# Optimization experiments

Measured on AMD Instinct MI355X. Metric: run time of the kernel, lower is better.

## Reference

```python
import jax, jax.numpy as jnp
import numpy as np

PAD = 7                 # init padding
T = 2 * PAD + 1         # T_side_dense = 15 shifts per axis
LAMDA = 1.0             # init lamda
EPS = 1e-16             # hardcoded epsilon in the torch loss body


def _joint_hist(x_out, x_tf_out):
    # Equivalent of F.conv2d(x_out.permute(1,0,2,3), weight=x_tf_out.permute(1,0,2,3), padding=PAD)
    # expressed as T*T shifted matmuls (correlation / cost-volume form).
    bn, k, h, w = x_out.shape
    A = jnp.transpose(x_out, (1, 0, 2, 3))      # (k, bn, h, w)  conv "input"
    B = jnp.transpose(x_tf_out, (1, 0, 2, 3))   # (k, bn, h, w)  conv "weight"
    A_pad = jnp.pad(A, ((0, 0), (0, 0), (PAD, PAD), (PAD, PAD)))

    def step(carry, s):
        dy, dx = s // T, s % T
        sl = jax.lax.dynamic_slice(A_pad, (0, 0, dy, dx), (k, bn, h, w))
        # p[n, o] at this shift = sum_{c,y,x} A_pad[n,c,y+dy,x+dx] * B[o,c,y,x]
        return carry, jnp.einsum('nchw,ochw->no', sl, B)

    _, p = jax.lax.scan(step, None, jnp.arange(T * T))
    # (T*T, k, k) -> (T, T, k, k); matches torch p_i_j.permute(2, 3, 0, 1)
    return p.reshape(T, T, k, k)


def reference(x_out, x_tf_out):
    p = _joint_hist(x_out, x_tf_out)
    # shift to positive; min is detached in torch -> stop_gradient
    p = p - jax.lax.stop_gradient(p.min()) + EPS
    # normalize per shift over the (k, k) joint
    p = p / p.sum(axis=(2, 3), keepdims=True)
    # symmetrize
    p = (p + jnp.swapaxes(p, 2, 3)) / 2.0
    p_i = p.sum(axis=2, keepdims=True)   # (T, T, 1, k) marginal (broadcasts like repeat)
    p_j = p.sum(axis=3, keepdims=True)   # (T, T, k, 1) marginal
    loss = (-p * (jnp.log(p + EPS)
                  - LAMDA * jnp.log(p_i + EPS)
                  - LAMDA * jnp.log(p_j + EPS))).sum() / (T * T)
    return loss


def setup_inputs() -> dict:
    key = jax.random.key(0)
    k1, k2 = jax.random.split(key)
    bn, k, h, w = 16, 10, 224, 224
    # simplex over axis=1 is asserted by the torch module -> use softmax
    x_out = jax.nn.softmax(jax.random.normal(k1, (bn, k, h, w), dtype=jnp.float32), axis=1)
    x_tf_out = jax.nn.softmax(jax.random.normal(k2, (bn, k, h, w), dtype=jnp.float32), axis=1)
    return {"x_out": x_out, "x_tf_out": x_tf_out}
```

## Files before the change

kernel.cpp:

```cpp
#include <hip/hip_runtime.h>
#include <stdint.h>
#include <math.h>


#define PADV 7
#define TS 15
#define KCLS 10
#define HH 224
#define WW 224
#define MD 160
#define NCELL (MD*MD)
#define NBLK 512
#define TY 7
#define BSTRIDE 232
#define BPH 240
#define ADW 120
#define LEPS 1e-16

typedef __attribute__((ext_vector_type(4))) float f32x4;
typedef __attribute__((ext_vector_type(8))) short bf16x8;

__device__ __forceinline__ unsigned short f2bf(float f) {
  union { float f; uint32_t u; } v; v.f = f;
  return (unsigned short)((v.u + 0x7FFFu + ((v.u >> 16) & 1u)) >> 16);
}

__device__ __forceinline__ void glds16(const unsigned short* g, unsigned short* l) {
  __builtin_amdgcn_global_load_lds(
      (const __attribute__((address_space(1))) unsigned int*)g,
      (__attribute__((address_space(3))) unsigned int*)l, 16, 0, 0);
}

struct U5 { uint32_t u[5]; };

__device__ __forceinline__ void ldA5(const uint32_t* p, U5& d) {
  uint4 t;
  __builtin_memcpy(&t, p, 16);
  d.u[0] = t.x; d.u[1] = t.y; d.u[2] = t.z; d.u[3] = t.w;
  d.u[4] = p[4];
}

#define BPREP_BLOCKS 4350
#define APREP_BLOCKS 4200
__global__ __launch_bounds__(256)
void prep(const float* __restrict__ xo, const float* __restrict__ xt,
          unsigned short* __restrict__ bp, uint32_t* __restrict__ ap) {
  if (blockIdx.x < BPREP_BLOCKS) {
    const int idx   = blockIdx.x * 256 + threadIdx.x;
    const int rowid = idx / 29;
    const int chunk = idx - rowid * 29;
    const int x0    = chunk * 8;
    const int yy    = rowid % BPH;
    const int cls   = rowid / BPH;
    const int row   = yy - PADV;
    union { unsigned short h[8]; uint4 v; } out;
    if (row >= 0 && row < HH && x0 < WW) {
      const float* src = xt + ((size_t)cls * HH + row) * WW + x0;
#pragma unroll
      for (int j = 0; j < 8; ++j) out.h[j] = f2bf(src[j]);
    } else {
      out.v = make_uint4(0u, 0u, 0u, 0u);
    }
    *(uint4*)(bp + (size_t)rowid * BSTRIDE + x0) = out.v;
  } else {
    const int idx   = (blockIdx.x - BPREP_BLOCKS) * 256 + threadIdx.x;
    const int rowid = idx / 30;
    const int wg    = idx - rowid * 30;
    const float* src = xo + (size_t)rowid * WW;
    float e[8];
#pragma unroll
    for (int j = 0; j < 8; ++j) {
      const int x = 8 * wg + j - PADV;
      e[j] = (x >= 0 && x < WW) ? src[x] : 0.f;
    }
    union { uint32_t u[4]; uint4 v; } o;
#pragma unroll
    for (int k = 0; k < 4; ++k)
      o.u[k] = (uint32_t)f2bf(e[2 * k]) | ((uint32_t)f2bf(e[2 * k + 1]) << 16);
    *(uint4*)(ap + (size_t)rowid * ADW + 4 * wg) = o.v;
  }
}

__global__ __launch_bounds__(256, 2)
void corr_gemm(const uint32_t* __restrict__ apad,
               const unsigned short* __restrict__ bpad,
               float* __restrict__ partials) {
  __shared__ __align__(16) unsigned short ldsB[KCLS * 16 * BSTRIDE];

  const int tid  = threadIdx.x;
  const int bid  = blockIdx.x;
  const int b    = bid >> 5;
  const int y0   = (bid & 31) * TY;

  const int lane = tid & 63;
  const int wv   = tid >> 6;
  const int wm   = wv & 1;
  const int wn   = wv >> 1;
  const int quad = lane >> 4;
  const int l15  = lane & 15;

  const int shA    = (l15 & 1) << 4;
  const int laneWd = quad * 4 + (l15 >> 1);

  f32x4 acc[5][5];
#pragma unroll
  for (int i = 0; i < 5; ++i)
#pragma unroll
    for (int j = 0; j < 5; ++j) acc[i][j] = (f32x4){0.f, 0.f, 0.f, 0.f};

  const unsigned short* Bb = bpad + (size_t)b * KCLS * BPH * BSTRIDE;
  const uint32_t* Abase = apad + ((size_t)(b * KCLS + wm * 5) * HH) * ADW;

  for (int pr = wv; pr < 15 * KCLS; pr += 4) {
    const int r15  = pr / KCLS;
    const int o    = pr - r15 * KCLS;
    const int yy   = y0 + r15;
    const int slot = (y0 - PADV + r15) & 15;
    if (lane < 29)
      glds16(Bb + ((size_t)o * BPH + yy) * BSTRIDE + lane * 8,
             ldsB + (o * 16 + slot) * BSTRIDE);
  }

  U5 bufA[5], bufB[5];
#pragma unroll
  for (int mi = 0; mi < 5; ++mi)
    ldA5(Abase + ((size_t)mi * HH + y0) * ADW + laneWd, bufA[mi]);

  __syncthreads();

  auto step = [&](int t, U5 (&use)[5], U5 (&pre)[5]) {
    const int ydiv = t / 7;
    const int xc   = t - 7 * ydiv;
    const int y    = y0 + ydiv;

    if (xc == 0) {
      const int yy   = y + 8 + PADV;
      const int slot = (y + 8) & 15;
      for (int ro = wv; ro < KCLS; ro += 4) {
        if (lane < 29)
          glds16(Bb + ((size_t)ro * BPH + yy) * BSTRIDE + lane * 8,
                 ldsB + (ro * 16 + slot) * BSTRIDE);
      }
    }

    if (t < 48) {
      const int t1    = t + 1;
      const int ydiv1 = t1 / 7;
      const int xc1   = t1 - 7 * ydiv1;
      const int y1    = y0 + ydiv1;
#pragma unroll
      for (int mi = 0; mi < 5; ++mi)
        ldA5(Abase + ((size_t)mi * HH + y1) * ADW + xc1 * 16 + laneWd, pre[mi]);
    }

    bf16x8 afrag[5];
#pragma unroll
    for (int mi = 0; mi < 5; ++mi) {
      union { uint32_t u[4]; bf16x8 v; } cv;
      cv.u[0] = __builtin_amdgcn_alignbit(use[mi].u[1], use[mi].u[0], shA);
      cv.u[1] = __builtin_amdgcn_alignbit(use[mi].u[2], use[mi].u[1], shA);
      cv.u[2] = __builtin_amdgcn_alignbit(use[mi].u[3], use[mi].u[2], shA);
      cv.u[3] = __builtin_amdgcn_alignbit(use[mi].u[4], use[mi].u[3], shA);
      afrag[mi] = cv.v;
    }

    const int x0    = xc * 32;
    const int slotB = (y + PADV - l15) & 15;
    bf16x8 bfrag[5];
#pragma unroll
    for (int ni = 0; ni < 5; ++ni) {
      const int to = wn * 5 + ni;
      bfrag[ni] = *(const bf16x8*)(ldsB + (to * 16 + slotB) * BSTRIDE + x0 + quad * 8);
    }

#pragma unroll
    for (int mi = 0; mi < 5; ++mi)
#pragma unroll
      for (int ni = 0; ni < 5; ++ni)
        acc[mi][ni] = __builtin_amdgcn_mfma_f32_16x16x32_bf16(
            afrag[mi], bfrag[ni], acc[mi][ni], 0, 0, 0);

    if (xc == 6 && t < 48) __syncthreads();
  };

  for (int ph = 0; ph < 25; ++ph) {
    const int t0 = 2 * ph;
    step(t0, bufA, bufB);
    if (t0 + 1 < 49) step(t0 + 1, bufB, bufA);
  }

  float* outp = partials + (size_t)bid * NCELL;
#pragma unroll
  for (int mi = 0; mi < 5; ++mi)
#pragma unroll
    for (int ni = 0; ni < 5; ++ni) {
      const int mrow = (wm * 5 + mi) * 16 + quad * 4;
      const int ncol = (wn * 5 + ni) * 16 + l15;
#pragma unroll
      for (int r = 0; r < 4; ++r)
        outp[(size_t)(mrow + r) * MD + ncol] = acc[mi][ni][r];
    }
}

__global__ __launch_bounds__(256)
void reduce_all(const float* __restrict__ partials, float* __restrict__ Cout,
                float* __restrict__ mins, float* __restrict__ dout) {
  const int c = blockIdx.x * 256 + threadIdx.x;
  if (c == 0) dout[0] = 0.f;
  double s0 = 0.0, s1 = 0.0, s2 = 0.0, s3 = 0.0;
  const float* base = partials + c;
  for (int p = 0; p < NBLK; p += 4) {
    s0 += (double)base[(size_t)(p + 0) * NCELL];
    s1 += (double)base[(size_t)(p + 1) * NCELL];
    s2 += (double)base[(size_t)(p + 2) * NCELL];
    s3 += (double)base[(size_t)(p + 3) * NCELL];
  }
  const float sf = (float)((s0 + s1) + (s2 + s3));
  Cout[c] = sf;
  const int m  = c / MD;
  const int nn = c - m * MD;
  const bool valid = ((m & 15) < TS) && ((nn & 15) < TS);
  __shared__ float red[256];
  red[threadIdx.x] = valid ? sf : 3.4e38f;
  __syncthreads();
  for (int st = 128; st > 0; st >>= 1) {
    if (threadIdx.x < st)
      red[threadIdx.x] = fminf(red[threadIdx.x], red[threadIdx.x + st]);
    __syncthreads();
  }
  if (threadIdx.x == 0) mins[blockIdx.x] = red[0];
}

__global__ __launch_bounds__(128)
void loss_kernel(const float* __restrict__ Cmat, const float* __restrict__ mins,
                 float* __restrict__ dout) {
  const int s   = blockIdx.x;
  const int dy  = s / TS;
  const int dx  = s - dy * TS;
  const int tid = threadIdx.x;
  __shared__ float fm[128];
  __shared__ double q[100];
  __shared__ double sym[100];
  __shared__ double pi[10], pj[10];
  __shared__ double red[128];

  fm[tid] = (tid < 100) ? mins[tid] : 3.4e38f;
  __syncthreads();
  for (int st = 64; st > 0; st >>= 1) {
    if (tid < st) fm[tid] = fminf(fm[tid], fm[tid + st]);
    __syncthreads();
  }
  const double minv = (double)fm[0];
  __syncthreads();

  if (tid < 100) {
    const int n = tid / 10, o = tid - (tid / 10) * 10;
    const double v = (double)Cmat[(size_t)(n * 16 + dx) * MD + (o * 16 + dy)];
    q[tid] = v - minv + LEPS;
  }
  __syncthreads();
  red[tid] = (tid < 100) ? q[tid] : 0.0;
  __syncthreads();
  for (int st = 64; st > 0; st >>= 1) {
    if (tid < st) red[tid] += red[tid + st];
    __syncthreads();
  }
  const double Z = red[0];
  __syncthreads();
  if (tid < 100) {
    const int n = tid / 10, o = tid - (tid / 10) * 10;
    sym[tid] = (q[n * 10 + o] + q[o * 10 + n]) * 0.5 / Z;
  }
  __syncthreads();
  if (tid < 10) {
    double a = 0.0, bsum = 0.0;
    for (int n2 = 0; n2 < 10; ++n2) {
      a    += sym[n2 * 10 + tid];
      bsum += sym[tid * 10 + n2];
    }
    pi[tid] = a;
    pj[tid] = bsum;
  }
  __syncthreads();
  double term = 0.0;
  if (tid < 100) {
    const int n = tid / 10, o = tid - (tid / 10) * 10;
    const double sp = sym[tid];
    term = -sp * (log(sp + LEPS) - log(pi[o] + LEPS) - log(pj[n] + LEPS));
  }
  red[tid] = term;
  __syncthreads();
  for (int st = 64; st > 0; st >>= 1) {
    if (tid < st) red[tid] += red[tid + st];
    __syncthreads();
  }
  if (tid == 0) atomicAdd(dout, (float)(red[0] / (double)(TS * TS)));
}

extern "C" void kernel_launch(void* const* d_in, const int* in_sizes, int n_in,
                              void* d_out, int out_size, void* d_ws, size_t ws_size,
                              hipStream_t stream) {
  const float* xo = (const float*)d_in[0];
  const float* xt = (const float*)d_in[1];
  float* ws       = (float*)d_ws;

  float* partials = ws;
  float* Cmat     = partials + (size_t)NBLK * NCELL;
  float* mins     = Cmat + NCELL;
  unsigned short* bpad = (unsigned short*)(mins + 128);
  uint32_t* apad  = (uint32_t*)(bpad + (size_t)160 * BPH * BSTRIDE);
  float* out      = (float*)d_out;

  hipLaunchKernelGGL(prep,       dim3(BPREP_BLOCKS + APREP_BLOCKS), dim3(256), 0, stream,
                     xo, xt, bpad, apad);
  hipLaunchKernelGGL(corr_gemm,  dim3(NBLK), dim3(256), 0, stream, apad, bpad, partials);
  hipLaunchKernelGGL(reduce_all, dim3(100),  dim3(256), 0, stream, partials, Cmat, mins, out);
  hipLaunchKernelGGL(loss_kernel,dim3(225),  dim3(128), 0, stream, Cmat, mins, out);
}
```

Before: 179.1 us.

## Split GEMM K-dimension across wave groups, halve blocks, parallelize partial reduction

The correlation GEMM now runs 512-thread blocks covering 14 output rows each. Two wave groups split the x-chunks between them, even and odd, and one group also issues the B-row DMA. Their accumulators are combined through LDS before a single partial write, which halves the partials buffer. The reduction kernel spreads each cell's partial sums over four thread groups across 400 blocks and uses a wave-shuffle minimum. The cost is LDS exchange traffic and an extra sync, plus lower occupancy from one 512-thread block per CU.

```diff
diff --git a/kernel.cpp b/kernel.cpp
--- a/kernel.cpp
+++ b/kernel.cpp
@@ -10,8 +10,8 @@
 #define WW 224
 #define MD 160
 #define NCELL (MD*MD)
-#define NBLK 512
-#define TY 7
+#define NBLK 256
+#define TY 14
 #define BSTRIDE 232
 #define BPH 240
 #define ADW 120
@@ -81,7 +81,7 @@
   }
 }
 
-__global__ __launch_bounds__(256, 2)
+__global__ __launch_bounds__(512, 1)
 void corr_gemm(const uint32_t* __restrict__ apad,
                const unsigned short* __restrict__ bpad,
                float* __restrict__ partials) {
@@ -89,13 +89,14 @@
 
   const int tid  = threadIdx.x;
   const int bid  = blockIdx.x;
-  const int b    = bid >> 5;
-  const int y0   = (bid & 31) * TY;
+  const int b    = bid >> 4;
+  const int y0   = (bid & 15) * TY;
 
   const int lane = tid & 63;
   const int wv   = tid >> 6;
   const int wm   = wv & 1;
-  const int wn   = wv >> 1;
+  const int wn   = (wv >> 1) & 1;
+  const int kw   = wv >> 2;
   const int quad = lane >> 4;
   const int l15  = lane & 15;
 
@@ -111,7 +112,7 @@
   const unsigned short* Bb = bpad + (size_t)b * KCLS * BPH * BSTRIDE;
   const uint32_t* Abase = apad + ((size_t)(b * KCLS + wm * 5) * HH) * ADW;
 
-  for (int pr = wv; pr < 15 * KCLS; pr += 4) {
+  for (int pr = wv; pr < 15 * KCLS; pr += 8) {
     const int r15  = pr / KCLS;
     const int o    = pr - r15 * KCLS;
     const int yy   = y0 + r15;
@@ -124,35 +125,17 @@
   U5 bufA[5], bufB[5];
 #pragma unroll
   for (int mi = 0; mi < 5; ++mi)
-    ldA5(Abase + ((size_t)mi * HH + y0) * ADW + laneWd, bufA[mi]);
-
-  __syncthreads();
-
-  auto step = [&](int t, U5 (&use)[5], U5 (&pre)[5]) {
-    const int ydiv = t / 7;
-    const int xc   = t - 7 * ydiv;
-    const int y    = y0 + ydiv;
-
-    if (xc == 0) {
-      const int yy   = y + 8 + PADV;
-      const int slot = (y + 8) & 15;
-      for (int ro = wv; ro < KCLS; ro += 4) {
-        if (lane < 29)
-          glds16(Bb + ((size_t)ro * BPH + yy) * BSTRIDE + lane * 8,
-                 ldsB + (ro * 16 + slot) * BSTRIDE);
-      }
-    }
-
-    if (t < 48) {
-      const int t1    = t + 1;
-      const int ydiv1 = t1 / 7;
-      const int xc1   = t1 - 7 * ydiv1;
-      const int y1    = y0 + ydiv1;
+    ldA5(Abase + ((size_t)mi * HH + y0) * ADW + kw * 16 + laneWd, bufA[mi]);
+
+  __syncthreads();
+
+  auto stepf = [&](int y, int xc, U5 (&use)[5], U5 (&pre)[5],
+                   int pny, int pnxc, bool dopre) {
+    if (dopre) {
 #pragma unroll
       for (int mi = 0; mi < 5; ++mi)
-        ldA5(Abase + ((size_t)mi * HH + y1) * ADW + xc1 * 16 + laneWd, pre[mi]);
-    }
-
+        ldA5(Abase + ((size_t)mi * HH + pny) * ADW + pnxc * 16 + laneWd, pre[mi]);
+    }
     bf16x8 afrag[5];
 #pragma unroll
     for (int mi = 0; mi < 5; ++mi) {
@@ -163,7 +146,6 @@
       cv.u[3] = __builtin_amdgcn_alignbit(use[mi].u[4], use[mi].u[3], shA);
       afrag[mi] = cv.v;
     }
-
     const int x0    = xc * 32;
     const int slotB = (y + PADV - l15) & 15;
     bf16x8 bfrag[5];
@@ -172,63 +154,127 @@
       const int to = wn * 5 + ni;
       bfrag[ni] = *(const bf16x8*)(ldsB + (to * 16 + slotB) * BSTRIDE + x0 + quad * 8);
     }
-
 #pragma unroll
     for (int mi = 0; mi < 5; ++mi)
 #pragma unroll
       for (int ni = 0; ni < 5; ++ni)
         acc[mi][ni] = __builtin_amdgcn_mfma_f32_16x16x32_bf16(
             afrag[mi], bfrag[ni], acc[mi][ni], 0, 0, 0);
-
-    if (xc == 6 && t < 48) __syncthreads();
   };
 
-  for (int ph = 0; ph < 25; ++ph) {
-    const int t0 = 2 * ph;
-    step(t0, bufA, bufB);
-    if (t0 + 1 < 49) step(t0 + 1, bufB, bufA);
-  }
-
+  auto dmaB = [&](int y) {
+    const int yy   = y + 15;
+    const int slot = (y + 8) & 15;
+    for (int ro = wv - 4; ro < KCLS; ro += 4)
+      if (lane < 29)
+        glds16(Bb + ((size_t)ro * BPH + yy) * BSTRIDE + lane * 8,
+               ldsB + (ro * 16 + slot) * BSTRIDE);
+  };
+
+  if (kw == 0) {
+#pragma unroll 1
+    for (int iy = 0; iy < TY; ++iy) {
+      const int y = y0 + iy;
+      const bool lastY = (iy == TY - 1);
+      stepf(y, 0, bufA, bufB, y, 2, true);
+      stepf(y, 2, bufB, bufA, y, 4, true);
+      stepf(y, 4, bufA, bufB, y, 6, true);
+      stepf(y, 6, bufB, bufA, y + 1, 0, !lastY);
+      if (!lastY) __syncthreads();
+    }
+  } else {
+#pragma unroll 1
+    for (int iy2 = 0; iy2 < TY; iy2 += 2) {
+      {
+        const int y = y0 + iy2;
+        dmaB(y);
+        stepf(y, 1, bufA, bufB, y, 3, true);
+        stepf(y, 3, bufB, bufA, y, 5, true);
+        stepf(y, 5, bufA, bufB, y + 1, 1, true);
+        __syncthreads();
+      }
+      {
+        const int iy = iy2 + 1;
+        const int y  = y0 + iy;
+        const bool lastY = (iy == TY - 1);
+        if (!lastY) dmaB(y);
+        stepf(y, 1, bufB, bufA, y, 3, true);
+        stepf(y, 3, bufA, bufB, y, 5, true);
+        stepf(y, 5, bufB, bufA, y + 1, 1, !lastY);
+        if (!lastY) __syncthreads();
+      }
+    }
+  }
+
+  __syncthreads();
+  float* ex = (float*)ldsB;
+  const int w1 = wm * 2 + wn;
   float* outp = partials + (size_t)bid * NCELL;
 #pragma unroll
-  for (int mi = 0; mi < 5; ++mi)
-#pragma unroll
-    for (int ni = 0; ni < 5; ++ni) {
-      const int mrow = (wm * 5 + mi) * 16 + quad * 4;
-      const int ncol = (wn * 5 + ni) * 16 + l15;
-#pragma unroll
-      for (int r = 0; r < 4; ++r)
-        outp[(size_t)(mrow + r) * MD + ncol] = acc[mi][ni][r];
-    }
+  for (int rd = 0; rd < 2; ++rd) {
+    const int mib = (rd == 0) ? 0 : 3;
+    const int nmi = (rd == 0) ? 3 : 2;
+    if (kw == 1) {
+#pragma unroll
+      for (int dmi = 0; dmi < 3; ++dmi) {
+        if (dmi >= nmi) break;
+#pragma unroll
+        for (int ni = 0; ni < 5; ++ni)
+          *(f32x4*)(ex + (((w1 * 3 + dmi) * 5 + ni) << 8) + lane * 4) =
+              acc[mib + dmi][ni];
+      }
+    }
+    __syncthreads();
+    if (kw == 0) {
+#pragma unroll
+      for (int dmi = 0; dmi < 3; ++dmi) {
+        if (dmi >= nmi) break;
+        const int mi = mib + dmi;
+#pragma unroll
+        for (int ni = 0; ni < 5; ++ni) {
+          const f32x4 other = *(const f32x4*)(ex + (((w1 * 3 + dmi) * 5 + ni) << 8) + lane * 4);
+          const int mrow = (wm * 5 + mi) * 16 + quad * 4;
+          const int ncol = (wn * 5 + ni) * 16 + l15;
+#pragma unroll
+          for (int r = 0; r < 4; ++r)
+            outp[(size_t)(mrow + r) * MD + ncol] = acc[mi][ni][r] + other[r];
+        }
+      }
+    }
+    __syncthreads();
+  }
 }
 
 __global__ __launch_bounds__(256)
 void reduce_all(const float* __restrict__ partials, float* __restrict__ Cout,
                 float* __restrict__ mins, float* __restrict__ dout) {
-  const int c = blockIdx.x * 256 + threadIdx.x;
-  if (c == 0) dout[0] = 0.f;
-  double s0 = 0.0, s1 = 0.0, s2 = 0.0, s3 = 0.0;
+  const int blk = blockIdx.x;
+  const int t   = threadIdx.x;
+  const int c   = blk * 64 + (t & 63);
+  const int ps  = t >> 6;
+  if (blk == 0 && t == 0) dout[0] = 0.f;
+  double s0 = 0.0, s1 = 0.0;
   const float* base = partials + c;
-  for (int p = 0; p < NBLK; p += 4) {
-    s0 += (double)base[(size_t)(p + 0) * NCELL];
+  for (int p = ps * 64; p < ps * 64 + 64; p += 2) {
+    s0 += (double)base[(size_t)p * NCELL];
     s1 += (double)base[(size_t)(p + 1) * NCELL];
-    s2 += (double)base[(size_t)(p + 2) * NCELL];
-    s3 += (double)base[(size_t)(p + 3) * NCELL];
-  }
-  const float sf = (float)((s0 + s1) + (s2 + s3));
-  Cout[c] = sf;
-  const int m  = c / MD;
-  const int nn = c - m * MD;
-  const bool valid = ((m & 15) < TS) && ((nn & 15) < TS);
-  __shared__ float red[256];
-  red[threadIdx.x] = valid ? sf : 3.4e38f;
-  __syncthreads();
-  for (int st = 128; st > 0; st >>= 1) {
-    if (threadIdx.x < st)
-      red[threadIdx.x] = fminf(red[threadIdx.x], red[threadIdx.x + st]);
-    __syncthreads();
-  }
-  if (threadIdx.x == 0) mins[blockIdx.x] = red[0];
+  }
+  __shared__ double red[256];
+  red[t] = s0 + s1;
+  __syncthreads();
+  if (t < 64) {
+    const double tot = red[t] + red[t + 64] + red[t + 128] + red[t + 192];
+    const float sf = (float)tot;
+    Cout[c] = sf;
+    const int m  = c / MD;
+    const int nn = c - m * MD;
+    const bool valid = ((m & 15) < TS) && ((nn & 15) < TS);
+    float v = valid ? sf : 3.4e38f;
+#pragma unroll
+    for (int off = 32; off > 0; off >>= 1)
+      v = fminf(v, __shfl_down(v, off));
+    if (t == 0) mins[blk] = v;
+  }
 }
 
 __global__ __launch_bounds__(128)
@@ -244,7 +290,9 @@
   __shared__ double pi[10], pj[10];
   __shared__ double red[128];
 
-  fm[tid] = (tid < 100) ? mins[tid] : 3.4e38f;
+  float v = 3.4e38f;
+  for (int i = tid; i < 400; i += 128) v = fminf(v, mins[i]);
+  fm[tid] = v;
   __syncthreads();
   for (int st = 64; st > 0; st >>= 1) {
     if (tid < st) fm[tid] = fminf(fm[tid], fm[tid + st]);
@@ -255,8 +303,8 @@
 
   if (tid < 100) {
     const int n = tid / 10, o = tid - (tid / 10) * 10;
-    const double v = (double)Cmat[(size_t)(n * 16 + dx) * MD + (o * 16 + dy)];
-    q[tid] = v - minv + LEPS;
+    const double vv = (double)Cmat[(size_t)(n * 16 + dx) * MD + (o * 16 + dy)];
+    q[tid] = vv - minv + LEPS;
   }
   __syncthreads();
   red[tid] = (tid < 100) ? q[tid] : 0.0;
@@ -307,13 +355,13 @@
   float* partials = ws;
   float* Cmat     = partials + (size_t)NBLK * NCELL;
   float* mins     = Cmat + NCELL;
-  unsigned short* bpad = (unsigned short*)(mins + 128);
+  unsigned short* bpad = (unsigned short*)(mins + 512);
   uint32_t* apad  = (uint32_t*)(bpad + (size_t)160 * BPH * BSTRIDE);
   float* out      = (float*)d_out;
 
   hipLaunchKernelGGL(prep,       dim3(BPREP_BLOCKS + APREP_BLOCKS), dim3(256), 0, stream,
                      xo, xt, bpad, apad);
-  hipLaunchKernelGGL(corr_gemm,  dim3(NBLK), dim3(256), 0, stream, apad, bpad, partials);
-  hipLaunchKernelGGL(reduce_all, dim3(100),  dim3(256), 0, stream, partials, Cmat, mins, out);
-  hipLaunchKernelGGL(loss_kernel,dim3(225),  dim3(128), 0, stream, Cmat, mins, out);
-}
+  hipLaunchKernelGGL(corr_gemm,  dim3(256), dim3(512), 0, stream, apad, bpad, partials);
+  hipLaunchKernelGGL(reduce_all, dim3(400), dim3(256), 0, stream, partials, Cmat, mins, out);
+  hipLaunchKernelGGL(loss_kernel,dim3(225), dim3(128), 0, stream, Cmat, mins, out);
+}
```

Result: faster. 166.4 us (-7.1%).

## Accumulate GEMM tiles via atomics and triple-buffer A fragment prefetch

Applied to the files above, without the earlier changes.

Replaces the per-block partials buffer (512 x 25600 floats) and the double-precision cross-block reduction with float atomic adds straight into a zeroed Cmat. The reduce kernel becomes a min-only pass. It also restructures the inner loop into a fully unrolled per-row body with three rotating A register buffers that prefetch two steps ahead. Float atomics give summation in a nondeterministic order and lose the double-precision accumulation. They also add atomic contention on 25600 cells across 512 blocks.

```diff
diff --git a/kernel.cpp b/kernel.cpp
--- a/kernel.cpp
+++ b/kernel.cpp
@@ -10,8 +10,6 @@
 #define WW 224
 #define MD 160
 #define NCELL (MD*MD)
-#define NBLK 512
-#define TY 7
 #define BSTRIDE 232
 #define BPH 240
 #define ADW 120
@@ -32,13 +30,6 @@
 }
 
 struct U5 { uint32_t u[5]; };
-
-__device__ __forceinline__ void ldA5(const uint32_t* p, U5& d) {
-  uint4 t;
-  __builtin_memcpy(&t, p, 16);
-  d.u[0] = t.x; d.u[1] = t.y; d.u[2] = t.z; d.u[3] = t.w;
-  d.u[4] = p[4];
-}
 
 #define BPREP_BLOCKS 4350
 #define APREP_BLOCKS 4200
@@ -84,13 +75,13 @@
 __global__ __launch_bounds__(256, 2)
 void corr_gemm(const uint32_t* __restrict__ apad,
                const unsigned short* __restrict__ bpad,
-               float* __restrict__ partials) {
+               float* __restrict__ Cmat) {
   __shared__ __align__(16) unsigned short ldsB[KCLS * 16 * BSTRIDE];
 
   const int tid  = threadIdx.x;
   const int bid  = blockIdx.x;
   const int b    = bid >> 5;
-  const int y0   = (bid & 31) * TY;
+  const int y0   = (bid & 31) * 7;
 
   const int lane = tid & 63;
   const int wv   = tid >> 6;
@@ -98,8 +89,7 @@
   const int wn   = wv >> 1;
   const int quad = lane >> 4;
   const int l15  = lane & 15;
-
-  const int shA    = (l15 & 1) << 4;
+  const int shA  = (l15 & 1) << 4;
   const int laneWd = quad * 4 + (l15 >> 1);
 
   f32x4 acc[5][5];
@@ -109,7 +99,11 @@
     for (int j = 0; j < 5; ++j) acc[i][j] = (f32x4){0.f, 0.f, 0.f, 0.f};
 
   const unsigned short* Bb = bpad + (size_t)b * KCLS * BPH * BSTRIDE;
-  const uint32_t* Abase = apad + ((size_t)(b * KCLS + wm * 5) * HH) * ADW;
+
+  const uint32_t* PA[5];
+#pragma unroll
+  for (int mi = 0; mi < 5; ++mi)
+    PA[mi] = apad + ((size_t)(b * KCLS + wm * 5 + mi) * HH + y0) * ADW + laneWd;
 
   for (int pr = wv; pr < 15 * KCLS; pr += 4) {
     const int r15  = pr / KCLS;
@@ -121,75 +115,79 @@
              ldsB + (o * 16 + slot) * BSTRIDE);
   }
 
-  U5 bufA[5], bufB[5];
-#pragma unroll
-  for (int mi = 0; mi < 5; ++mi)
-    ldA5(Abase + ((size_t)mi * HH + y0) * ADW + laneWd, bufA[mi]);
-
-  __syncthreads();
-
-  auto step = [&](int t, U5 (&use)[5], U5 (&pre)[5]) {
-    const int ydiv = t / 7;
-    const int xc   = t - 7 * ydiv;
-    const int y    = y0 + ydiv;
-
-    if (xc == 0) {
-      const int yy   = y + 8 + PADV;
+  U5 b0[5], b1[5], b2[5];
+
+  auto fetchA = [&](U5 (&dst)[5], int dyi, int xc) {
+#pragma unroll
+    for (int mi = 0; mi < 5; ++mi) {
+      const uint32_t* p = PA[mi] + dyi * ADW + xc * 16;
+      uint4 t;
+      __builtin_memcpy(&t, p, 16);
+      dst[mi].u[0] = t.x; dst[mi].u[1] = t.y;
+      dst[mi].u[2] = t.z; dst[mi].u[3] = t.w;
+      dst[mi].u[4] = p[4];
+    }
+  };
+
+  auto computeS = [&](U5 (&buf)[5], int slotB, int xc) {
+    bf16x8 afrag[5], bfrag[5];
+#pragma unroll
+    for (int mi = 0; mi < 5; ++mi) {
+      union { uint32_t u[4]; bf16x8 v; } cv;
+      cv.u[0] = __builtin_amdgcn_alignbit(buf[mi].u[1], buf[mi].u[0], shA);
+      cv.u[1] = __builtin_amdgcn_alignbit(buf[mi].u[2], buf[mi].u[1], shA);
+      cv.u[2] = __builtin_amdgcn_alignbit(buf[mi].u[3], buf[mi].u[2], shA);
+      cv.u[3] = __builtin_amdgcn_alignbit(buf[mi].u[4], buf[mi].u[3], shA);
+      afrag[mi] = cv.v;
+    }
+#pragma unroll
+    for (int ni = 0; ni < 5; ++ni) {
+      const int to = wn * 5 + ni;
+      bfrag[ni] = *(const bf16x8*)(ldsB + (to * 16 + slotB) * BSTRIDE + xc * 32 + quad * 8);
+    }
+#pragma unroll
+    for (int mi = 0; mi < 5; ++mi)
+#pragma unroll
+      for (int ni = 0; ni < 5; ++ni)
+        acc[mi][ni] = __builtin_amdgcn_mfma_f32_16x16x32_bf16(
+            afrag[mi], bfrag[ni], acc[mi][ni], 0, 0, 0);
+  };
+
+  auto ybody = [&](U5 (&p0)[5], U5 (&p1)[5], U5 (&p2)[5], int y, int dyi, bool last) {
+    if (!last) {
+      const int yy   = y + 15;
       const int slot = (y + 8) & 15;
-      for (int ro = wv; ro < KCLS; ro += 4) {
+      for (int ro = wv; ro < KCLS; ro += 4)
         if (lane < 29)
           glds16(Bb + ((size_t)ro * BPH + yy) * BSTRIDE + lane * 8,
                  ldsB + (ro * 16 + slot) * BSTRIDE);
-      }
-    }
-
-    if (t < 48) {
-      const int t1    = t + 1;
-      const int ydiv1 = t1 / 7;
-      const int xc1   = t1 - 7 * ydiv1;
-      const int y1    = y0 + ydiv1;
-#pragma unroll
-      for (int mi = 0; mi < 5; ++mi)
-        ldA5(Abase + ((size_t)mi * HH + y1) * ADW + xc1 * 16 + laneWd, pre[mi]);
-    }
-
-    bf16x8 afrag[5];
-#pragma unroll
-    for (int mi = 0; mi < 5; ++mi) {
-      union { uint32_t u[4]; bf16x8 v; } cv;
-      cv.u[0] = __builtin_amdgcn_alignbit(use[mi].u[1], use[mi].u[0], shA);
-      cv.u[1] = __builtin_amdgcn_alignbit(use[mi].u[2], use[mi].u[1], shA);
-      cv.u[2] = __builtin_amdgcn_alignbit(use[mi].u[3], use[mi].u[2], shA);
-      cv.u[3] = __builtin_amdgcn_alignbit(use[mi].u[4], use[mi].u[3], shA);
-      afrag[mi] = cv.v;
-    }
-
-    const int x0    = xc * 32;
+    }
     const int slotB = (y + PADV - l15) & 15;
-    bf16x8 bfrag[5];
-#pragma unroll
-    for (int ni = 0; ni < 5; ++ni) {
-      const int to = wn * 5 + ni;
-      bfrag[ni] = *(const bf16x8*)(ldsB + (to * 16 + slotB) * BSTRIDE + x0 + quad * 8);
-    }
-
-#pragma unroll
-    for (int mi = 0; mi < 5; ++mi)
-#pragma unroll
-      for (int ni = 0; ni < 5; ++ni)
-        acc[mi][ni] = __builtin_amdgcn_mfma_f32_16x16x32_bf16(
-            afrag[mi], bfrag[ni], acc[mi][ni], 0, 0, 0);
-
-    if (xc == 6 && t < 48) __syncthreads();
+    fetchA(p2, dyi, 2);               computeS(p0, slotB, 0);
+    fetchA(p0, dyi, 3);               computeS(p1, slotB, 1);
+    fetchA(p1, dyi, 4);               computeS(p2, slotB, 2);
+    fetchA(p2, dyi, 5);               computeS(p0, slotB, 3);
+    fetchA(p0, dyi, 6);               computeS(p1, slotB, 4);
+    if (!last) fetchA(p1, dyi + 1, 0); computeS(p2, slotB, 5);
+    if (!last) fetchA(p2, dyi + 1, 1); computeS(p0, slotB, 6);
+    if (!last) __syncthreads();
   };
 
-  for (int ph = 0; ph < 25; ++ph) {
-    const int t0 = 2 * ph;
-    step(t0, bufA, bufB);
-    if (t0 + 1 < 49) step(t0 + 1, bufB, bufA);
-  }
-
-  float* outp = partials + (size_t)bid * NCELL;
+  fetchA(b0, 0, 0);
+  fetchA(b1, 0, 1);
+  __syncthreads();
+
+#pragma unroll 1
+  for (int k = 0; k < 2; ++k) {
+    const int yb = y0 + 3 * k;
+    ybody(b0, b1, b2, yb + 0, 0, false);
+    ybody(b1, b2, b0, yb + 1, 1, false);
+    ybody(b2, b0, b1, yb + 2, 2, false);
+#pragma unroll
+    for (int mi = 0; mi < 5; ++mi) PA[mi] += 3 * ADW;
+  }
+  ybody(b0, b1, b2, y0 + 6, 0, true);
+
 #pragma unroll
   for (int mi = 0; mi < 5; ++mi)
 #pragma unroll
@@ -198,25 +196,14 @@
       const int ncol = (wn * 5 + ni) * 16 + l15;
 #pragma unroll
       for (int r = 0; r < 4; ++r)
-        outp[(size_t)(mrow + r) * MD + ncol] = acc[mi][ni][r];
+        unsafeAtomicAdd(&Cmat[(size_t)(mrow + r) * MD + ncol], acc[mi][ni][r]);
     }
 }
 
 __global__ __launch_bounds__(256)
-void reduce_all(const float* __restrict__ partials, float* __restrict__ Cout,
-                float* __restrict__ mins, float* __restrict__ dout) {
+void minred(const float* __restrict__ Cmat, float* __restrict__ mins) {
   const int c = blockIdx.x * 256 + threadIdx.x;
-  if (c == 0) dout[0] = 0.f;
-  double s0 = 0.0, s1 = 0.0, s2 = 0.0, s3 = 0.0;
-  const float* base = partials + c;
-  for (int p = 0; p < NBLK; p += 4) {
-    s0 += (double)base[(size_t)(p + 0) * NCELL];
-    s1 += (double)base[(size_t)(p + 1) * NCELL];
-    s2 += (double)base[(size_t)(p + 2) * NCELL];
-    s3 += (double)base[(size_t)(p + 3) * NCELL];
-  }
-  const float sf = (float)((s0 + s1) + (s2 + s3));
-  Cout[c] = sf;
+  const float sf = Cmat[c];
   const int m  = c / MD;
   const int nn = c - m * MD;
   const bool valid = ((m & 15) < TS) && ((nn & 15) < TS);
@@ -255,8 +242,8 @@
 
   if (tid < 100) {
     const int n = tid / 10, o = tid - (tid / 10) * 10;
-    const double v = (double)Cmat[(size_t)(n * 16 + dx) * MD + (o * 16 + dy)];
-    q[tid] = v - minv + LEPS;
+    const double vv = (double)Cmat[(size_t)(n * 16 + dx) * MD + (o * 16 + dy)];
+    q[tid] = vv - minv + LEPS;
   }
   __syncthreads();
   red[tid] = (tid < 100) ? q[tid] : 0.0;
@@ -304,16 +291,17 @@
   const float* xt = (const float*)d_in[1];
   float* ws       = (float*)d_ws;
 
-  float* partials = ws;
-  float* Cmat     = partials + (size_t)NBLK * NCELL;
+  float* Cmat     = ws;
   float* mins     = Cmat + NCELL;
   unsigned short* bpad = (unsigned short*)(mins + 128);
   uint32_t* apad  = (uint32_t*)(bpad + (size_t)160 * BPH * BSTRIDE);
   float* out      = (float*)d_out;
 
+  hipMemsetAsync(Cmat, 0, (size_t)NCELL * sizeof(float), stream);
+  hipMemsetAsync(out, 0, sizeof(float), stream);
   hipLaunchKernelGGL(prep,       dim3(BPREP_BLOCKS + APREP_BLOCKS), dim3(256), 0, stream,
                      xo, xt, bpad, apad);
-  hipLaunchKernelGGL(corr_gemm,  dim3(NBLK), dim3(256), 0, stream, apad, bpad, partials);
-  hipLaunchKernelGGL(reduce_all, dim3(100),  dim3(256), 0, stream, partials, Cmat, mins, out);
-  hipLaunchKernelGGL(loss_kernel,dim3(225),  dim3(128), 0, stream, Cmat, mins, out);
-}
+  hipLaunchKernelGGL(corr_gemm,  dim3(512), dim3(256), 0, stream, apad, bpad, Cmat);
+  hipLaunchKernelGGL(minred,     dim3(100), dim3(256), 0, stream, Cmat, mins);
+  hipLaunchKernelGGL(loss_kernel,dim3(225), dim3(128), 0, stream, Cmat, mins, out);
+}
```

Measured after the change: 216.6 us. 20.9% more time.
